# Kernel optimization log

Hardware: AMD Instinct MI355X
Metric: run time of the kernel (lower is better)

The kernel has to match this reference:

```python
import jax, jax.numpy as jnp
import numpy as np

F = 64  # n_atom_basis


def setup_inputs() -> dict:
    key = jax.random.key(0)
    ks = jax.random.split(key, 10)
    n_atoms = 20000
    n_pairs = 640000
    q = jax.random.normal(ks[0], (n_atoms, 1, F), dtype=jnp.float32)
    mu = jax.random.normal(ks[1], (n_atoms, 3, F), dtype=jnp.float32)
    Wij = jax.random.normal(ks[2], (n_pairs, 1, 3 * F), dtype=jnp.float32)
    dir_ij = jax.random.normal(ks[3], (n_pairs, 3), dtype=jnp.float32)
    idx_i = jnp.sort(jax.random.randint(ks[4], (n_pairs,), 0, n_atoms))
    idx_j = jax.random.randint(ks[5], (n_pairs,), 0, n_atoms)
    # intra_atomic_net: Linear(F,F) + SiLU, then Linear(F, 3F)
    s1 = 1.0 / np.sqrt(F)
    W1 = jax.random.uniform(ks[6], (F, F), jnp.float32, -s1, s1)
    b1 = jax.random.uniform(ks[7], (F,), jnp.float32, -s1, s1)
    W2 = jax.random.uniform(ks[8], (F, 3 * F), jnp.float32, -s1, s1)
    b2 = jax.random.uniform(ks[9], (3 * F,), jnp.float32, -s1, s1)
    return {"q": q, "mu": mu, "Wij": Wij, "dir_ij": dir_ij,
            "idx_i": idx_i, "idx_j": idx_j, "n_atoms": n_atoms,
            "W1": W1, "b1": b1, "W2": W2, "b2": b2}


def reference(q, mu, Wij, dir_ij, idx_i, idx_j, n_atoms, W1, b1, W2, b2):
    # intra-atomic MLP: [N,1,F] -> [N,1,3F]
    x = jax.nn.silu(q @ W1 + b1) @ W2 + b2
    # gather neighbor features
    xj = x[idx_j]          # [P,1,3F]
    muj = mu[idx_j]        # [P,3,F]
    x = Wij * xj           # elementwise filter, [P,1,3F]
    dq, dmuR, dmumu = jnp.split(x, 3, axis=-1)  # each [P,1,F]
    dq = jax.ops.segment_sum(dq, idx_i, num_segments=n_atoms)  # [N,1,F]
    dmu = dmuR * dir_ij[..., None] + dmumu * muj                # [P,3,F]
    dmu = jax.ops.segment_sum(dmu, idx_i, num_segments=n_atoms)  # [N,3,F]
    return q + dq, mu + dmu
```

## Files before the change

kernel.cpp:

```cpp
#include <hip/hip_runtime.h>

#define F 64
#define F3 192
#define XMW 384

typedef unsigned short ushort_t;
typedef unsigned int   u32;
typedef ushort_t us4 __attribute__((ext_vector_type(4)));

__device__ __forceinline__ float bf2f(ushort_t u) {
    return __uint_as_float((unsigned)u << 16);
}
__device__ __forceinline__ ushort_t f2bf(float v) {
    unsigned b = __float_as_uint(v);
    return (ushort_t)((b + 0x7FFFu + ((b >> 16) & 1u)) >> 16);
}

__global__ __launch_bounds__(256) void mlp_kernel(
    const float* __restrict__ q, const float* __restrict__ mu,
    const float* __restrict__ W1, const float* __restrict__ b1,
    const float* __restrict__ W2, const float* __restrict__ b2,
    ushort_t* __restrict__ xmu, int N)
{
    __shared__ float W2s[F * F3];
    __shared__ float b1s[F];
    __shared__ float b2s[F3];
    __shared__ float qs[4 * F];
    __shared__ float hs[4 * F];

    const int t = threadIdx.x;
    for (int i = t; i < F * F3; i += 256) W2s[i] = W2[i];
    if (t < F)  b1s[t] = b1[t];
    if (t < F3) b2s[t] = b2[t];
    __syncthreads();

    const int a = t >> 6;
    const int f = t & 63;
    const int ngroups = (N + 3) >> 2;

    for (int g = blockIdx.x; g < ngroups; g += gridDim.x) {
        const int atom = g * 4 + a;
        qs[t] = (atom < N) ? q[atom * F + f] : 0.f;
        __syncthreads();

        float h = b1s[f];
        #pragma unroll
        for (int k = 0; k < F; ++k)
            h = fmaf(qs[a * F + k], W1[k * F + f], h);
        h = h / (1.f + __expf(-h));
        hs[t] = h;
        __syncthreads();

        float acc0 = b2s[f], acc1 = b2s[F + f], acc2 = b2s[2 * F + f];
        #pragma unroll
        for (int k = 0; k < F; ++k) {
            const float hk = hs[a * F + k];
            acc0 = fmaf(hk, W2s[k * F3 + f],         acc0);
            acc1 = fmaf(hk, W2s[k * F3 + F + f],     acc1);
            acc2 = fmaf(hk, W2s[k * F3 + 2 * F + f], acc2);
        }
        if (atom < N) {
            ushort_t* r = xmu + (size_t)atom * XMW;
            const float* mi = mu + (size_t)atom * F3;
            us4 va;
            va.x = f2bf(acc0);
            va.y = f2bf(acc1);
            va.z = f2bf(acc2);
            va.w = f2bf(mi[f]);
            ((us4*)r)[f] = va;
            const u32 ub = (u32)f2bf(mi[F + f]) | ((u32)f2bf(mi[2 * F + f]) << 16);
            ((u32*)(r + 256))[f] = ub;
        }
        __syncthreads();
    }
}

__global__ void rowstart_kernel(const int* __restrict__ idx_i,
                                int* __restrict__ row_start, int P, int N)
{
    const int p = blockIdx.x * blockDim.x + threadIdx.x;
    if (p > P) return;
    if (p == P) {
        const int prev = idx_i[P - 1];
        for (int n = prev + 1; n <= N; ++n) row_start[n] = P;
    } else {
        const int cur  = idx_i[p];
        const int prev = (p == 0) ? -1 : idx_i[p - 1];
        for (int n = prev + 1; n <= cur; ++n) row_start[n] = p;
    }
}

__global__ __launch_bounds__(256) void accum_kernel(
    const float* __restrict__ q, const float* __restrict__ mu,
    const float* __restrict__ Wij, const float* __restrict__ dir_ij,
    const int* __restrict__ idx_j, const int* __restrict__ row_start,
    const ushort_t* __restrict__ xmu, float* __restrict__ out, int N)
{
    const int a = blockIdx.x * 4 + (threadIdx.x >> 6);
    const int f = threadIdx.x & 63;
    if (a >= N) return;

    const int start = __builtin_amdgcn_readfirstlane(row_start[a]);
    const int end   = __builtin_amdgcn_readfirstlane(row_start[a + 1]);

    float dq = 0.f, dm0 = 0.f, dm1 = 0.f, dm2 = 0.f;

    #pragma unroll 4
    for (int p = start; p < end; ++p) {
        const int j = __builtin_amdgcn_readfirstlane(idx_j[p]);

        const float*    wp = Wij + (size_t)p * F3;
        const ushort_t* r  = xmu + (size_t)j * XMW;

        const float wq = __builtin_nontemporal_load(wp + f);
        const float wr = __builtin_nontemporal_load(wp + F + f);
        const float wm = __builtin_nontemporal_load(wp + 2 * F + f);

        const us4 va = ((const us4*)r)[f];
        const u32 ub = ((const u32*)(r + 256))[f];

        const float xq = bf2f(va.x);
        const float xr = bf2f(va.y);
        const float xm = bf2f(va.z);
        const float m0 = bf2f(va.w);
        const float m1 = bf2f((ushort_t)(ub & 0xFFFFu));
        const float m2 = bf2f((ushort_t)(ub >> 16));

        const float d0 = dir_ij[p * 3 + 0];
        const float d1 = dir_ij[p * 3 + 1];
        const float d2 = dir_ij[p * 3 + 2];

        dq = fmaf(wq, xq, dq);
        const float vr = wr * xr;
        const float vm = wm * xm;
        dm0 = fmaf(vr, d0, fmaf(vm, m0, dm0));
        dm1 = fmaf(vr, d1, fmaf(vm, m1, dm1));
        dm2 = fmaf(vr, d2, fmaf(vm, m2, dm2));
    }

    out[(size_t)a * F + f] = __builtin_nontemporal_load(q + (size_t)a * F + f) + dq;
    float*       om = out + (size_t)N * F + (size_t)a * F3;
    const float* mi = mu  + (size_t)a * F3;
    om[f]         = __builtin_nontemporal_load(mi + f)         + dm0;
    om[F + f]     = __builtin_nontemporal_load(mi + F + f)     + dm1;
    om[2 * F + f] = __builtin_nontemporal_load(mi + 2 * F + f) + dm2;
}

extern "C" void kernel_launch(void* const* d_in, const int* in_sizes, int n_in,
                              void* d_out, int out_size, void* d_ws, size_t ws_size,
                              hipStream_t stream)
{
    const float* q      = (const float*)d_in[0];
    const float* mu     = (const float*)d_in[1];
    const float* Wij    = (const float*)d_in[2];
    const float* dir_ij = (const float*)d_in[3];
    const int*   idx_i  = (const int*)d_in[4];
    const int*   idx_j  = (const int*)d_in[5];
    const float* W1     = (const float*)d_in[7];
    const float* b1     = (const float*)d_in[8];
    const float* W2     = (const float*)d_in[9];
    const float* b2     = (const float*)d_in[10];

    const int N = in_sizes[0] / F;
    const int P = in_sizes[2] / F3;

    char* w = (char*)d_ws;
    size_t o = 0;
    ushort_t* xmu = (ushort_t*)(w + o);    o += (size_t)N * XMW * sizeof(ushort_t);
    o = (o + 255) & ~(size_t)255;
    int* row_start = (int*)(w + o);        o += (size_t)(N + 1) * sizeof(int);

    float* out = (float*)d_out;

    mlp_kernel<<<1280, 256, 0, stream>>>(q, mu, W1, b1, W2, b2, xmu, N);
    rowstart_kernel<<<(P + 1 + 255) / 256, 256, 0, stream>>>(idx_i, row_start, P, N);
    accum_kernel<<<(N + 3) / 4, 256, 0, stream>>>(q, mu, Wij, dir_ij, idx_j,
                                                  row_start, xmu, out, N);
}
```

Before: 183.0 us.

## Bucket neighbor pairs by source-atom slice to localize xmu gathers

Adds a bucketing pass that reorders each atom's pairs into NS=8 slices by idx_j range. Each slice is accumulated by its own block, interleaved so that blocks running at the same time hit a narrower region of the gathered xmu table and get better cache locality. Partial sums are written in bf16 and combined in a separate reduce kernel. This costs two extra kernels, an index indirection, extra partial-buffer traffic and more bf16 rounding error in the sums.

```diff
diff --git a/kernel.cpp b/kernel.cpp
--- a/kernel.cpp
+++ b/kernel.cpp
@@ -3,6 +3,7 @@
 #define F 64
 #define F3 192
 #define XMW 384
+#define NS 8
 
 typedef unsigned short ushort_t;
 typedef unsigned int   u32;
@@ -90,23 +91,57 @@
     }
 }
 
-__global__ __launch_bounds__(256) void accum_kernel(
-    const float* __restrict__ q, const float* __restrict__ mu,
+__global__ __launch_bounds__(64) void bucket_kernel(
+    const int* __restrict__ idx_j, const int* __restrict__ row_start,
+    int* __restrict__ ord, int* __restrict__ cs, int N)
+{
+    __shared__ int soff[64][NS + 1];
+    const int t = threadIdx.x;
+    const int a = blockIdx.x * 64 + t;
+    if (a >= N) return;
+    const int s0 = row_start[a], s1 = row_start[a + 1];
+
+    for (int s = 0; s < NS; ++s) soff[t][s] = 0;
+    for (int p = s0; p < s1; ++p) {
+        const int j = idx_j[p];
+        const int s = (int)(((long long)j * NS) / N);
+        soff[t][s]++;
+    }
+    int off = s0;
+    for (int s = 0; s < NS; ++s) {
+        const int c = soff[t][s];
+        cs[a * (NS + 1) + s] = off;
+        soff[t][s] = off;
+        off += c;
+    }
+    cs[a * (NS + 1) + NS] = off;
+    for (int p = s0; p < s1; ++p) {
+        const int j = idx_j[p];
+        const int s = (int)(((long long)j * NS) / N);
+        ord[soff[t][s]++] = p;
+    }
+}
+
+__global__ __launch_bounds__(256) void slice_accum_kernel(
     const float* __restrict__ Wij, const float* __restrict__ dir_ij,
-    const int* __restrict__ idx_j, const int* __restrict__ row_start,
-    const ushort_t* __restrict__ xmu, float* __restrict__ out, int N)
-{
-    const int a = blockIdx.x * 4 + (threadIdx.x >> 6);
+    const int* __restrict__ idx_j, const int* __restrict__ ord,
+    const int* __restrict__ cs, const ushort_t* __restrict__ xmu,
+    ushort_t* __restrict__ partial, int N)
+{
+    const int s = blockIdx.x & (NS - 1);
+    const int g = blockIdx.x >> 3;
+    const int a = g * 4 + (threadIdx.x >> 6);
     const int f = threadIdx.x & 63;
     if (a >= N) return;
 
-    const int start = __builtin_amdgcn_readfirstlane(row_start[a]);
-    const int end   = __builtin_amdgcn_readfirstlane(row_start[a + 1]);
+    const int p0 = __builtin_amdgcn_readfirstlane(cs[a * (NS + 1) + s]);
+    const int p1 = __builtin_amdgcn_readfirstlane(cs[a * (NS + 1) + s + 1]);
 
     float dq = 0.f, dm0 = 0.f, dm1 = 0.f, dm2 = 0.f;
 
-    #pragma unroll 4
-    for (int p = start; p < end; ++p) {
+    #pragma unroll 2
+    for (int pp = p0; pp < p1; ++pp) {
+        const int p = __builtin_amdgcn_readfirstlane(ord[pp]);
         const int j = __builtin_amdgcn_readfirstlane(idx_j[p]);
 
         const float*    wp = Wij + (size_t)p * F3;
@@ -138,12 +173,40 @@
         dm2 = fmaf(vr, d2, fmaf(vm, m2, dm2));
     }
 
-    out[(size_t)a * F + f] = __builtin_nontemporal_load(q + (size_t)a * F + f) + dq;
+    us4 v;
+    v.x = f2bf(dq);
+    v.y = f2bf(dm0);
+    v.z = f2bf(dm1);
+    v.w = f2bf(dm2);
+    ushort_t* pr = partial + ((size_t)s * N + a) * 256;
+    __builtin_nontemporal_store(v, (us4*)pr + f);
+}
+
+__global__ __launch_bounds__(256) void reduce_kernel(
+    const float* __restrict__ q, const float* __restrict__ mu,
+    const ushort_t* __restrict__ partial, float* __restrict__ out, int N)
+{
+    const int a = blockIdx.x * 4 + (threadIdx.x >> 6);
+    const int f = threadIdx.x & 63;
+    if (a >= N) return;
+
+    float dq = 0.f, dm0 = 0.f, dm1 = 0.f, dm2 = 0.f;
+    #pragma unroll
+    for (int s = 0; s < NS; ++s) {
+        const us4 v = __builtin_nontemporal_load(
+            (const us4*)(partial + ((size_t)s * N + a) * 256) + f);
+        dq  += bf2f(v.x);
+        dm0 += bf2f(v.y);
+        dm1 += bf2f(v.z);
+        dm2 += bf2f(v.w);
+    }
+
+    out[(size_t)a * F + f] = q[(size_t)a * F + f] + dq;
     float*       om = out + (size_t)N * F + (size_t)a * F3;
     const float* mi = mu  + (size_t)a * F3;
-    om[f]         = __builtin_nontemporal_load(mi + f)         + dm0;
-    om[F + f]     = __builtin_nontemporal_load(mi + F + f)     + dm1;
-    om[2 * F + f] = __builtin_nontemporal_load(mi + 2 * F + f) + dm2;
+    om[f]         = mi[f]         + dm0;
+    om[F + f]     = mi[F + f]     + dm1;
+    om[2 * F + f] = mi[2 * F + f] + dm2;
 }
 
 extern "C" void kernel_launch(void* const* d_in, const int* in_sizes, int n_in,
@@ -169,11 +232,20 @@
     ushort_t* xmu = (ushort_t*)(w + o);    o += (size_t)N * XMW * sizeof(ushort_t);
     o = (o + 255) & ~(size_t)255;
     int* row_start = (int*)(w + o);        o += (size_t)(N + 1) * sizeof(int);
+    o = (o + 255) & ~(size_t)255;
+    int* ord = (int*)(w + o);              o += (size_t)P * sizeof(int);
+    o = (o + 255) & ~(size_t)255;
+    int* cs = (int*)(w + o);               o += (size_t)N * (NS + 1) * sizeof(int);
+    o = (o + 255) & ~(size_t)255;
+    ushort_t* partial = (ushort_t*)(w + o); o += (size_t)NS * N * 256 * sizeof(ushort_t);
 
     float* out = (float*)d_out;
+    const int ngroups = (N + 3) / 4;
 
     mlp_kernel<<<1280, 256, 0, stream>>>(q, mu, W1, b1, W2, b2, xmu, N);
     rowstart_kernel<<<(P + 1 + 255) / 256, 256, 0, stream>>>(idx_i, row_start, P, N);
-    accum_kernel<<<(N + 3) / 4, 256, 0, stream>>>(q, mu, Wij, dir_ij, idx_j,
-                                                  row_start, xmu, out, N);
-}
+    bucket_kernel<<<(N + 63) / 64, 64, 0, stream>>>(idx_j, row_start, ord, cs, N);
+    slice_accum_kernel<<<ngroups * NS, 256, 0, stream>>>(Wij, dir_ij, idx_j, ord,
+                                                         cs, xmu, partial, N);
+    reduce_kernel<<<ngroups, 256, 0, stream>>>(q, mu, partial, out, N);
+}
```

Measured after the change: 218.6 us. 19.4% more time.
